# Kernel optimization log

Measured on AMD Instinct MI355X. Metric: run time of the kernel, lower is better.

Reference implementation:

```python
import jax, jax.numpy as jnp
import numpy as np

B, S, D, H = 8, 1024, 768, 12
DH = D // H  # per-head dim = 64


def setup_inputs() -> dict:
    key = jax.random.key(0)
    ks = jax.random.split(key, 9)
    scale = 1.0 / np.sqrt(D)
    x = jax.random.normal(ks[0], (B, S, D), dtype=jnp.float32)
    # Per-head projection weights stacked over the head axis [H, D, DH]
    Wq = jax.random.normal(ks[1], (H, D, DH), dtype=jnp.float32) * scale
    bq = jax.random.normal(ks[2], (H, DH), dtype=jnp.float32) * 0.02
    Wk = jax.random.normal(ks[3], (H, D, DH), dtype=jnp.float32) * scale
    bk = jax.random.normal(ks[4], (H, DH), dtype=jnp.float32) * 0.02
    Wv = jax.random.normal(ks[5], (H, D, DH), dtype=jnp.float32) * scale
    bv = jax.random.normal(ks[6], (H, DH), dtype=jnp.float32) * 0.02
    Wo = jax.random.normal(ks[7], (D, D), dtype=jnp.float32) * scale
    bo = jax.random.normal(ks[8], (D,), dtype=jnp.float32) * 0.02
    return {"x": x, "Wq": Wq, "bq": bq, "Wk": Wk, "bk": bk,
            "Wv": Wv, "bv": bv, "Wo": Wo, "bo": bo}


def reference(x, Wq, bq, Wk, bk, Wv, bv, Wo, bo):
    # Batched equivalent of the per-head Python loop: each head has its own
    # Q/K/V linear projections (weights stacked on the head axis).
    q = jnp.einsum('bsd,hde->bhse', x, Wq) + bq[None, :, None, :]
    k = jnp.einsum('bsd,hde->bhse', x, Wk) + bk[None, :, None, :]
    v = jnp.einsum('bsd,hde->bhse', x, Wv) + bv[None, :, None, :]
    scores = jnp.einsum('bhse,bhte->bhst', q, k) / jnp.sqrt(jnp.float32(DH))
    attn = jax.nn.softmax(scores, axis=-1)
    out = jnp.einsum('bhst,bhte->bhse', attn, v)  # [B,H,S,DH]
    # concat heads on last dim -> [B,S,H*DH] = [B,S,D]
    out = out.transpose(0, 2, 1, 3).reshape(B, S, D)
    return out @ Wo.T + bo
```

## Files before the change

### kernel.cpp

```cpp
#include <hip/hip_runtime.h>
#include <hip/hip_bf16.h>


typedef unsigned short u16;
typedef unsigned int u32;
typedef __attribute__((ext_vector_type(8))) short bf16x8;
typedef __attribute__((ext_vector_type(8))) unsigned short u16x8;
typedef __attribute__((ext_vector_type(4))) float f32x4;
typedef __attribute__((ext_vector_type(4))) u32 u32x4;

typedef __attribute__((address_space(1))) const u32* gas_u32;
typedef __attribute__((address_space(3))) u32* las_u32;

#define DEVI __device__ __forceinline__

DEVI u16 f2bf(float f) {
  union { float f; u32 u; } v; v.f = f;
  u32 r = v.u + 0x7fffu + ((v.u >> 16) & 1u);
  return (u16)(r >> 16);
}

DEVI void gll16(const void* g, void* l) {
  __builtin_amdgcn_global_load_lds((gas_u32)g, (las_u32)l, 16, 0, 0);
}

DEVI f32x4 mfma16(bf16x8 a, bf16x8 b, f32x4 c) {
  return __builtin_amdgcn_mfma_f32_16x16x32_bf16(a, b, c, 0, 0, 0);
}

DEVI u32 cvtpk(float lo, float hi) {
  u32 r;
  asm("v_cvt_pk_bf16_f32 %0, %1, %2" : "=v"(r) : "v"(lo), "v"(hi));
  return r;
}

__global__ __launch_bounds__(256) void k_prep(const float* __restrict__ x,
                                              u16* __restrict__ xb,
                                              const float* __restrict__ Wo,
                                              u16* __restrict__ Wob,
                                              const float* __restrict__ Wq,
                                              const float* __restrict__ Wk,
                                              const float* __restrict__ Wv,
                                              u16* __restrict__ Wtb) {
  __shared__ u16 T[64][65];
  const int blk = blockIdx.x;
  const int tid = threadIdx.x;
  if (blk < 6720) {
    const float* in; u16* out; int idx;
    if (blk < 6144) { in = x;  out = xb;  idx = blk * 256 + tid; }
    else            { in = Wo; out = Wob; idx = (blk - 6144) * 256 + tid; }
    float4 v = ((const float4*)in)[idx];
    ushort4 o;
    o.x = f2bf(v.x); o.y = f2bf(v.y); o.z = f2bf(v.z); o.w = f2bf(v.w);
    ((ushort4*)out)[idx] = o;
    return;
  }
  const int blk2 = blk - 6720;
  const int th = blk2 / 12;
  const int k0 = (blk2 % 12) * 64;
  const float* W = (th < 12) ? Wq : (th < 24) ? Wk : Wv;
  const int h = th % 12;
  W += (size_t)h * 768 * 64;
  const int row = tid >> 2, c = tid & 3;
  const float* src = W + (size_t)(k0 + row) * 64 + c * 16;
#pragma unroll
  for (int j = 0; j < 4; ++j) {
    float4 v = ((const float4*)src)[j];
    T[row][c * 16 + j * 4 + 0] = f2bf(v.x);
    T[row][c * 16 + j * 4 + 1] = f2bf(v.y);
    T[row][c * 16 + j * 4 + 2] = f2bf(v.z);
    T[row][c * 16 + j * 4 + 3] = f2bf(v.w);
  }
  __syncthreads();
  const int e = tid >> 2;
  u16* dst = Wtb + ((size_t)th * 64 + e) * 768 + k0 + c * 16;
  alignas(16) u16 tmp[16];
#pragma unroll
  for (int j = 0; j < 16; ++j) tmp[j] = T[c * 16 + j][e];
  *(u16x8*)(dst)     = *(const u16x8*)(tmp);
  *(u16x8*)(dst + 8) = *(const u16x8*)(tmp + 8);
}

__global__ __launch_bounds__(256) void k_gemmQKV(const u16* __restrict__ Ab,
                                                 const u16* __restrict__ Wtb,
                                                 const float* __restrict__ bq,
                                                 const float* __restrict__ bk,
                                                 const float* __restrict__ bv,
                                                 u16* __restrict__ Qb,
                                                 u16* __restrict__ VTb) {
  __shared__ u16 smem[12288];
  u16* As = smem;
  u16* Bs = smem + 128 * 64;
  const int tid = threadIdx.x;
  const int w = tid >> 6, lane = tid & 63, lq = lane & 15, g = lane >> 4;
  const int wm = w >> 1, wn = w & 1;
  const int m0 = blockIdx.x * 128;
  const int pn = blockIdx.y;
  const u16* Brows = Wtb + (size_t)pn * 64 * 768;

  f32x4 acc[4][2];
#pragma unroll
  for (int mf = 0; mf < 4; ++mf)
#pragma unroll
    for (int nf = 0; nf < 2; ++nf) acc[mf][nf] = (f32x4){0.f, 0.f, 0.f, 0.f};

  for (int kt = 0; kt < 12; ++kt) {
    const int kb = kt * 64;
#pragma unroll
    for (int i = 0; i < 4; ++i) {
      int c = w * 4 + i;
      int id = c * 64 + lane;
      int row = id >> 3, cb = id & 7;
      gll16(Ab + (size_t)(m0 + row) * 768 + kb + ((cb ^ (row & 7)) << 3), As + c * 512);
    }
#pragma unroll
    for (int i = 0; i < 2; ++i) {
      int c = w * 2 + i;
      int id = c * 64 + lane;
      int row = id >> 3, cb = id & 7;
      gll16(Brows + (size_t)row * 768 + kb + ((cb ^ (row & 7)) << 3), Bs + c * 512);
    }
    __syncthreads();
#pragma unroll
    for (int kk = 0; kk < 2; ++kk) {
      bf16x8 a[4], b[2];
#pragma unroll
      for (int mf = 0; mf < 4; ++mf) {
        int row = wm * 64 + mf * 16 + lq;
        a[mf] = *(const bf16x8*)(As + row * 64 + (((kk * 64 + g * 16) ^ ((row & 7) << 4)) >> 1));
      }
#pragma unroll
      for (int nf = 0; nf < 2; ++nf) {
        int row = wn * 32 + nf * 16 + lq;
        b[nf] = *(const bf16x8*)(Bs + row * 64 + (((kk * 64 + g * 16) ^ ((row & 7) << 4)) >> 1));
      }
#pragma unroll
      for (int mf = 0; mf < 4; ++mf)
#pragma unroll
        for (int nf = 0; nf < 2; ++nf)
          acc[mf][nf] = mfma16(a[mf], b[nf], acc[mf][nf]);
    }
    __syncthreads();
  }

  const int sel = pn / 12;
  const int ph  = pn % 12;
  const int b = m0 >> 10;
  if (sel == 2) {
    u16* Ct = smem;
#pragma unroll
    for (int nf = 0; nf < 2; ++nf) {
      const int e = wn * 32 + nf * 16 + lq;
      const float bi = bv[ph * 64 + e];
#pragma unroll
      for (int mf = 0; mf < 4; ++mf)
#pragma unroll
        for (int r = 0; r < 4; ++r) {
          int sl = wm * 64 + mf * 16 + 4 * g + r;
          Ct[e * 136 + sl] = f2bf(acc[mf][nf][r] + bi);
        }
    }
    __syncthreads();
    const int er = tid >> 2, cc = tid & 3;
    u16* dst = VTb + ((size_t)(b * 12 + ph) * 64 + er) * 1024 + (m0 & 1023) + cc * 32;
#pragma unroll
    for (int i = 0; i < 4; ++i)
      *(u16x8*)(dst + i * 8) = *(const u16x8*)(Ct + er * 136 + cc * 32 + i * 8);
  } else {
    u16* out = Qb + (size_t)sel * 6291456;
    const float qs = sel ? 1.0f : 0.18033688f;
    const float* bp = sel ? bk : bq;
#pragma unroll
    for (int nf = 0; nf < 2; ++nf) {
      const int e = wn * 32 + nf * 16 + lq;
      const float bi = bp[ph * 64 + e];
#pragma unroll
      for (int mf = 0; mf < 4; ++mf)
#pragma unroll
        for (int r = 0; r < 4; ++r) {
          int s = (m0 & 1023) + wm * 64 + mf * 16 + 4 * g + r;
          out[((size_t)(b * 12 + ph) * 1024 + s) * 64 + e] = f2bf((acc[mf][nf][r] + bi) * qs);
        }
    }
  }
}

__global__ __launch_bounds__(256) void k_gemmO(const u16* __restrict__ Ab,
                                               const u16* __restrict__ Bb,
                                               const float* __restrict__ bias,
                                               float* __restrict__ out) {
  __shared__ u16 smem[12288];
  u16* As = smem;
  u16* Bs = smem + 128 * 64;
  const int tid = threadIdx.x;
  const int w = tid >> 6, lane = tid & 63, lq = lane & 15, g = lane >> 4;
  const int wm = w >> 1, wn = w & 1;
  const int m0 = blockIdx.x * 128;
  const int pn = blockIdx.y;
  const u16* Brows = Bb + (size_t)pn * 64 * 768;

  f32x4 acc[4][2];
#pragma unroll
  for (int mf = 0; mf < 4; ++mf)
#pragma unroll
    for (int nf = 0; nf < 2; ++nf) acc[mf][nf] = (f32x4){0.f, 0.f, 0.f, 0.f};

  for (int kt = 0; kt < 12; ++kt) {
    const int kb = kt * 64;
#pragma unroll
    for (int i = 0; i < 4; ++i) {
      int c = w * 4 + i;
      int id = c * 64 + lane;
      int row = id >> 3, cb = id & 7;
      gll16(Ab + (size_t)(m0 + row) * 768 + kb + ((cb ^ (row & 7)) << 3), As + c * 512);
    }
#pragma unroll
    for (int i = 0; i < 2; ++i) {
      int c = w * 2 + i;
      int id = c * 64 + lane;
      int row = id >> 3, cb = id & 7;
      gll16(Brows + (size_t)row * 768 + kb + ((cb ^ (row & 7)) << 3), Bs + c * 512);
    }
    __syncthreads();
#pragma unroll
    for (int kk = 0; kk < 2; ++kk) {
      bf16x8 a[4], b[2];
#pragma unroll
      for (int mf = 0; mf < 4; ++mf) {
        int row = wm * 64 + mf * 16 + lq;
        a[mf] = *(const bf16x8*)(As + row * 64 + (((kk * 64 + g * 16) ^ ((row & 7) << 4)) >> 1));
      }
#pragma unroll
      for (int nf = 0; nf < 2; ++nf) {
        int row = wn * 32 + nf * 16 + lq;
        b[nf] = *(const bf16x8*)(Bs + row * 64 + (((kk * 64 + g * 16) ^ ((row & 7) << 4)) >> 1));
      }
#pragma unroll
      for (int mf = 0; mf < 4; ++mf)
#pragma unroll
        for (int nf = 0; nf < 2; ++nf)
          acc[mf][nf] = mfma16(a[mf], b[nf], acc[mf][nf]);
    }
    __syncthreads();
  }

#pragma unroll
  for (int nf = 0; nf < 2; ++nf) {
    const int n = pn * 64 + wn * 32 + nf * 16 + lq;
    const float bi = bias[n];
#pragma unroll
    for (int mf = 0; mf < 4; ++mf)
#pragma unroll
      for (int r = 0; r < 4; ++r) {
        int m = m0 + wm * 64 + mf * 16 + 4 * g + r;
        out[(size_t)m * 768 + n] = acc[mf][nf][r] + bi;
      }
  }
}

__global__ __launch_bounds__(512) void k_attn(const u16* __restrict__ Qb,
                                              const u16* __restrict__ Kb,
                                              const u16* __restrict__ VTb,
                                              u16* __restrict__ AO) {
  __shared__ u16 Ksm[2][4096];
  __shared__ u16 Vsm[2][4096];
  const int tid = threadIdx.x;
  const int w = tid >> 6, lane = tid & 63, lq = lane & 15, g = lane >> 4;
  const int bh = blockIdx.x, b = bh / 12, h = bh % 12;
  const int q0 = blockIdx.y * 128 + w * 16;
  const u16* Qw = Qb + ((size_t)bh * 1024 + q0) * 64;
  const u16* Kp = Kb + (size_t)bh * 65536;
  const u16* Vp = VTb + (size_t)bh * 65536;
  const bool gsel = (g & 1);

  bf16x8 qf[2];
#pragma unroll
  for (int kk = 0; kk < 2; ++kk)
    qf[kk] = *(const bf16x8*)(Qw + lq * 64 + kk * 32 + g * 8);

  f32x4 o[4];
#pragma unroll
  for (int ef = 0; ef < 4; ++ef) o[ef] = (f32x4){0.f, 0.f, 0.f, 0.f};
  float l_ = 0.f;

#define STAGE(buf, kt_)                                                          \
  {                                                                              \
    const int kb_ = (kt_) * 64;                                                  \
    const int id = w * 64 + lane;                                                \
    const int row = id >> 3, cb = id & 7;                                        \
    const int sb = cb ^ (row & 7);                                               \
    const int tb = (sb & 4) | ((sb & 1) << 1) | ((sb >> 1) & 1);                 \
    gll16(Kp + (size_t)(kb_ + row) * 64 + (sb << 3), &Ksm[buf][w * 512]);        \
    gll16(Vp + (size_t)row * 1024 + kb_ + (tb << 3), &Vsm[buf][w * 512]);        \
  }

#define TILE(buf)                                                                \
  {                                                                              \
    f32x4 s[4];                                                                  \
    _Pragma("unroll")                                                            \
    for (int kf = 0; kf < 4; ++kf) s[kf] = (f32x4){0.f, 0.f, 0.f, 0.f};          \
    __builtin_amdgcn_s_setprio(1);                                               \
    _Pragma("unroll")                                                            \
    for (int kf = 0; kf < 4; ++kf) {                                             \
      const int row = kf * 16 + lq;                                              \
      _Pragma("unroll")                                                          \
      for (int kk = 0; kk < 2; ++kk) {                                           \
        bf16x8 kfr = *(const bf16x8*)(&Ksm[buf][0] + row * 64 +                  \
                                      (((kk * 64 + g * 16) ^ ((row & 7) << 4)) >> 1)); \
        s[kf] = mfma16(kfr, qf[kk], s[kf]);                                      \
      }                                                                          \
    }                                                                            \
    __builtin_amdgcn_s_setprio(0);                                               \
    float sm = 0.f;                                                              \
    _Pragma("unroll")                                                            \
    for (int kf = 0; kf < 4; ++kf)                                               \
      _Pragma("unroll")                                                          \
      for (int r = 0; r < 4; ++r) {                                              \
        float p = __builtin_amdgcn_exp2f(s[kf][r]);                              \
        s[kf][r] = p;                                                            \
        sm += p;                                                                 \
      }                                                                          \
    l_ += sm;                                                                    \
    u32 D[4][2];                                                                 \
    _Pragma("unroll")                                                            \
    for (int kf = 0; kf < 4; ++kf) {                                             \
      D[kf][0] = cvtpk(s[kf][0], s[kf][1]);                                      \
      D[kf][1] = cvtpk(s[kf][2], s[kf][3]);                                      \
    }                                                                            \
    _Pragma("unroll")                                                            \
    for (int kk = 0; kk < 2; ++kk) {                                             \
      const int kk2 = kk * 2;                                                    \
      u32 sa0 = gsel ? D[kk2][0] : D[kk2 + 1][0];                                \
      u32 sa1 = gsel ? D[kk2][1] : D[kk2 + 1][1];                                \
      u32 xa0 = __shfl_xor(sa0, 16), xa1 = __shfl_xor(sa1, 16);                  \
      u32x4 t = { gsel ? xa0 : D[kk2][0],                                        \
                  gsel ? xa1 : D[kk2][1],                                        \
                  gsel ? D[kk2 + 1][0] : xa0,                                    \
                  gsel ? D[kk2 + 1][1] : xa1 };                                  \
      bf16x8 pb = __builtin_bit_cast(bf16x8, t);                                 \
      __builtin_amdgcn_s_setprio(1);                                             \
      _Pragma("unroll")                                                          \
      for (int ef = 0; ef < 4; ++ef) {                                           \
        const int row = ef * 16 + lq;                                            \
        bf16x8 vf = *(const bf16x8*)(&Vsm[buf][0] + row * 64 +                   \
                                     (((kk * 64 + g * 16) ^ ((row & 7) << 4)) >> 1)); \
        o[ef] = mfma16(vf, pb, o[ef]);                                           \
      }                                                                          \
      __builtin_amdgcn_s_setprio(0);                                             \
    }                                                                            \
  }

  STAGE(0, 0)
  asm volatile("s_waitcnt vmcnt(0)" ::: "memory");
  __syncthreads();

  for (int it = 0; it < 8; ++it) {
    const int kt = it * 2;
    STAGE(1, kt + 1)
    TILE(0)
    asm volatile("s_waitcnt vmcnt(0)" ::: "memory");
    __syncthreads();
    if (it < 7) STAGE(0, kt + 2)
    TILE(1)
    asm volatile("s_waitcnt vmcnt(0)" ::: "memory");
    __syncthreads();
  }

  l_ += __shfl_xor(l_, 16);
  l_ += __shfl_xor(l_, 32);

  const float inv = 1.0f / l_;
  u16* dst = AO + ((size_t)(b * 1024 + q0 + lq)) * 768 + h * 64 + g * 4;
#pragma unroll
  for (int ef = 0; ef < 4; ++ef) {
    ushort4 t;
    t.x = f2bf(o[ef][0] * inv);
    t.y = f2bf(o[ef][1] * inv);
    t.z = f2bf(o[ef][2] * inv);
    t.w = f2bf(o[ef][3] * inv);
    *(ushort4*)(dst + ef * 16) = t;
  }
#undef STAGE
#undef TILE
}

extern "C" void kernel_launch(void* const* d_in, const int* in_sizes, int n_in,
                              void* d_out, int out_size, void* d_ws, size_t ws_size,
                              hipStream_t stream) {
  (void)in_sizes; (void)n_in; (void)out_size; (void)ws_size;
  const float* x  = (const float*)d_in[0];
  const float* Wq = (const float*)d_in[1];
  const float* bq = (const float*)d_in[2];
  const float* Wk = (const float*)d_in[3];
  const float* bk = (const float*)d_in[4];
  const float* Wv = (const float*)d_in[5];
  const float* bv = (const float*)d_in[6];
  const float* Wo = (const float*)d_in[7];
  const float* bo = (const float*)d_in[8];

  char* ws = (char*)d_ws;
  u16* xb  = (u16*)(ws);
  u16* Wtb = (u16*)(ws + 12582912);
  u16* Wob = (u16*)(ws + 12582912 + 3538944);
  u16* Qb  = (u16*)(ws + 12582912 + 3538944 + 1179648);
  u16* Kb  = Qb + (size_t)96 * 1024 * 64;
  u16* VTb = Kb + (size_t)96 * 1024 * 64;
  u16* AO  = xb;

  k_prep<<<7152, 256, 0, stream>>>(x, xb, Wo, Wob, Wq, Wk, Wv, Wtb);

  k_gemmQKV<<<dim3(64, 36), 256, 0, stream>>>(xb, Wtb, bq, bk, bv, Qb, VTb);

  k_attn<<<dim3(96, 8), 512, 0, stream>>>(Qb, Kb, VTb, AO);

  k_gemmO<<<dim3(64, 12), 256, 0, stream>>>(AO, Wob, bo, (float*)d_out);
}
```

Before: 107.8 us.

## Double-buffer LDS tiles in QKV and output-projection GEMMs

Both projection GEMM kernels now keep two LDS stages and issue the async global-to-LDS loads for the next K tile before computing on the current one. This overlaps global memory latency with MFMA work and halves the barriers per K tile. In exchange, LDS per block doubles to 48KB, which may lower occupancy. The attention kernel is unchanged.

```diff
diff --git a/kernel.cpp b/kernel.cpp
--- a/kernel.cpp
+++ b/kernel.cpp
@@ -88,14 +88,13 @@
                                                  const float* __restrict__ bv,
                                                  u16* __restrict__ Qb,
                                                  u16* __restrict__ VTb) {
-  __shared__ u16 smem[12288];
-  u16* As = smem;
-  u16* Bs = smem + 128 * 64;
+  __shared__ u16 smem[2][12288];
   const int tid = threadIdx.x;
   const int w = tid >> 6, lane = tid & 63, lq = lane & 15, g = lane >> 4;
   const int wm = w >> 1, wn = w & 1;
   const int m0 = blockIdx.x * 128;
   const int pn = blockIdx.y;
+  const u16* Arows = Ab + (size_t)m0 * 768;
   const u16* Brows = Wtb + (size_t)pn * 64 * 768;
 
   f32x4 acc[4][2];
@@ -104,50 +103,76 @@
 #pragma unroll
     for (int nf = 0; nf < 2; ++nf) acc[mf][nf] = (f32x4){0.f, 0.f, 0.f, 0.f};
 
-  for (int kt = 0; kt < 12; ++kt) {
-    const int kb = kt * 64;
-#pragma unroll
-    for (int i = 0; i < 4; ++i) {
-      int c = w * 4 + i;
-      int id = c * 64 + lane;
-      int row = id >> 3, cb = id & 7;
-      gll16(Ab + (size_t)(m0 + row) * 768 + kb + ((cb ^ (row & 7)) << 3), As + c * 512);
-    }
-#pragma unroll
-    for (int i = 0; i < 2; ++i) {
-      int c = w * 2 + i;
-      int id = c * 64 + lane;
-      int row = id >> 3, cb = id & 7;
-      gll16(Brows + (size_t)row * 768 + kb + ((cb ^ (row & 7)) << 3), Bs + c * 512);
-    }
-    __syncthreads();
-#pragma unroll
-    for (int kk = 0; kk < 2; ++kk) {
-      bf16x8 a[4], b[2];
-#pragma unroll
-      for (int mf = 0; mf < 4; ++mf) {
-        int row = wm * 64 + mf * 16 + lq;
-        a[mf] = *(const bf16x8*)(As + row * 64 + (((kk * 64 + g * 16) ^ ((row & 7) << 4)) >> 1));
-      }
-#pragma unroll
-      for (int nf = 0; nf < 2; ++nf) {
-        int row = wn * 32 + nf * 16 + lq;
-        b[nf] = *(const bf16x8*)(Bs + row * 64 + (((kk * 64 + g * 16) ^ ((row & 7) << 4)) >> 1));
-      }
-#pragma unroll
-      for (int mf = 0; mf < 4; ++mf)
-#pragma unroll
-        for (int nf = 0; nf < 2; ++nf)
-          acc[mf][nf] = mfma16(a[mf], b[nf], acc[mf][nf]);
-    }
-    __syncthreads();
-  }
+#define QSTAGE(buf, kt_)                                                         \
+  {                                                                              \
+    const int kb_ = (kt_) * 64;                                                  \
+    _Pragma("unroll")                                                            \
+    for (int i = 0; i < 4; ++i) {                                                \
+      int c = w * 4 + i;                                                         \
+      int id = c * 64 + lane;                                                    \
+      int row = id >> 3, cb = id & 7;                                            \
+      gll16(Arows + (size_t)row * 768 + kb_ + ((cb ^ (row & 7)) << 3),           \
+            &smem[buf][c * 512]);                                                \
+    }                                                                            \
+    _Pragma("unroll")                                                            \
+    for (int i = 0; i < 2; ++i) {                                                \
+      int c = w * 2 + i;                                                         \
+      int id = c * 64 + lane;                                                    \
+      int row = id >> 3, cb = id & 7;                                            \
+      gll16(Brows + (size_t)row * 768 + kb_ + ((cb ^ (row & 7)) << 3),           \
+            &smem[buf][8192 + c * 512]);                                         \
+    }                                                                            \
+  }
+
+#define QCOMP(buf)                                                               \
+  {                                                                              \
+    const u16* As_ = &smem[buf][0];                                              \
+    const u16* Bs_ = &smem[buf][8192];                                           \
+    _Pragma("unroll")                                                            \
+    for (int kk = 0; kk < 2; ++kk) {                                             \
+      bf16x8 a[4], b[2];                                                         \
+      _Pragma("unroll")                                                          \
+      for (int mf = 0; mf < 4; ++mf) {                                           \
+        int row = wm * 64 + mf * 16 + lq;                                        \
+        a[mf] = *(const bf16x8*)(As_ + row * 64 +                                \
+                                 (((kk * 64 + g * 16) ^ ((row & 7) << 4)) >> 1)); \
+      }                                                                          \
+      _Pragma("unroll")                                                          \
+      for (int nf = 0; nf < 2; ++nf) {                                           \
+        int row = wn * 32 + nf * 16 + lq;                                        \
+        b[nf] = *(const bf16x8*)(Bs_ + row * 64 +                                \
+                                 (((kk * 64 + g * 16) ^ ((row & 7) << 4)) >> 1)); \
+      }                                                                          \
+      _Pragma("unroll")                                                          \
+      for (int mf = 0; mf < 4; ++mf)                                             \
+        _Pragma("unroll")                                                        \
+        for (int nf = 0; nf < 2; ++nf)                                           \
+          acc[mf][nf] = mfma16(a[mf], b[nf], acc[mf][nf]);                       \
+    }                                                                            \
+  }
+
+  QSTAGE(0, 0)
+  asm volatile("s_waitcnt vmcnt(0)" ::: "memory");
+  __syncthreads();
+  for (int it = 0; it < 6; ++it) {
+    const int kt = it * 2;
+    QSTAGE(1, kt + 1)
+    QCOMP(0)
+    asm volatile("s_waitcnt vmcnt(0)" ::: "memory");
+    __syncthreads();
+    if (it < 5) QSTAGE(0, kt + 2)
+    QCOMP(1)
+    asm volatile("s_waitcnt vmcnt(0)" ::: "memory");
+    __syncthreads();
+  }
+#undef QSTAGE
+#undef QCOMP
 
   const int sel = pn / 12;
   const int ph  = pn % 12;
   const int b = m0 >> 10;
   if (sel == 2) {
-    u16* Ct = smem;
+    u16* Ct = &smem[0][0];
 #pragma unroll
     for (int nf = 0; nf < 2; ++nf) {
       const int e = wn * 32 + nf * 16 + lq;
@@ -189,14 +214,13 @@
                                                const u16* __restrict__ Bb,
                                                const float* __restrict__ bias,
                                                float* __restrict__ out) {
-  __shared__ u16 smem[12288];
-  u16* As = smem;
-  u16* Bs = smem + 128 * 64;
+  __shared__ u16 smem[2][12288];
   const int tid = threadIdx.x;
   const int w = tid >> 6, lane = tid & 63, lq = lane & 15, g = lane >> 4;
   const int wm = w >> 1, wn = w & 1;
   const int m0 = blockIdx.x * 128;
   const int pn = blockIdx.y;
+  const u16* Arows = Ab + (size_t)m0 * 768;
   const u16* Brows = Bb + (size_t)pn * 64 * 768;
 
   f32x4 acc[4][2];
@@ -205,44 +229,70 @@
 #pragma unroll
     for (int nf = 0; nf < 2; ++nf) acc[mf][nf] = (f32x4){0.f, 0.f, 0.f, 0.f};
 
-  for (int kt = 0; kt < 12; ++kt) {
-    const int kb = kt * 64;
-#pragma unroll
-    for (int i = 0; i < 4; ++i) {
-      int c = w * 4 + i;
-      int id = c * 64 + lane;
-      int row = id >> 3, cb = id & 7;
-      gll16(Ab + (size_t)(m0 + row) * 768 + kb + ((cb ^ (row & 7)) << 3), As + c * 512);
-    }
-#pragma unroll
-    for (int i = 0; i < 2; ++i) {
-      int c = w * 2 + i;
-      int id = c * 64 + lane;
-      int row = id >> 3, cb = id & 7;
-      gll16(Brows + (size_t)row * 768 + kb + ((cb ^ (row & 7)) << 3), Bs + c * 512);
-    }
-    __syncthreads();
-#pragma unroll
-    for (int kk = 0; kk < 2; ++kk) {
-      bf16x8 a[4], b[2];
-#pragma unroll
-      for (int mf = 0; mf < 4; ++mf) {
-        int row = wm * 64 + mf * 16 + lq;
-        a[mf] = *(const bf16x8*)(As + row * 64 + (((kk * 64 + g * 16) ^ ((row & 7) << 4)) >> 1));
-      }
-#pragma unroll
-      for (int nf = 0; nf < 2; ++nf) {
-        int row = wn * 32 + nf * 16 + lq;
-        b[nf] = *(const bf16x8*)(Bs + row * 64 + (((kk * 64 + g * 16) ^ ((row & 7) << 4)) >> 1));
-      }
-#pragma unroll
-      for (int mf = 0; mf < 4; ++mf)
-#pragma unroll
-        for (int nf = 0; nf < 2; ++nf)
-          acc[mf][nf] = mfma16(a[mf], b[nf], acc[mf][nf]);
-    }
-    __syncthreads();
-  }
+#define OSTAGE(buf, kt_)                                                         \
+  {                                                                              \
+    const int kb_ = (kt_) * 64;                                                  \
+    _Pragma("unroll")                                                            \
+    for (int i = 0; i < 4; ++i) {                                                \
+      int c = w * 4 + i;                                                         \
+      int id = c * 64 + lane;                                                    \
+      int row = id >> 3, cb = id & 7;                                            \
+      gll16(Arows + (size_t)row * 768 + kb_ + ((cb ^ (row & 7)) << 3),           \
+            &smem[buf][c * 512]);                                                \
+    }                                                                            \
+    _Pragma("unroll")                                                            \
+    for (int i = 0; i < 2; ++i) {                                                \
+      int c = w * 2 + i;                                                         \
+      int id = c * 64 + lane;                                                    \
+      int row = id >> 3, cb = id & 7;                                            \
+      gll16(Brows + (size_t)row * 768 + kb_ + ((cb ^ (row & 7)) << 3),           \
+            &smem[buf][8192 + c * 512]);                                         \
+    }                                                                            \
+  }
+
+#define OCOMP(buf)                                                               \
+  {                                                                              \
+    const u16* As_ = &smem[buf][0];                                              \
+    const u16* Bs_ = &smem[buf][8192];                                           \
+    _Pragma("unroll")                                                            \
+    for (int kk = 0; kk < 2; ++kk) {                                             \
+      bf16x8 a[4], b[2];                                                         \
+      _Pragma("unroll")                                                          \
+      for (int mf = 0; mf < 4; ++mf) {                                           \
+        int row = wm * 64 + mf * 16 + lq;                                        \
+        a[mf] = *(const bf16x8*)(As_ + row * 64 +                                \
+                                 (((kk * 64 + g * 16) ^ ((row & 7) << 4)) >> 1)); \
+      }                                                                          \
+      _Pragma("unroll")                                                          \
+      for (int nf = 0; nf < 2; ++nf) {                                           \
+        int row = wn * 32 + nf * 16 + lq;                                        \
+        b[nf] = *(const bf16x8*)(Bs_ + row * 64 +                                \
+                                 (((kk * 64 + g * 16) ^ ((row & 7) << 4)) >> 1)); \
+      }                                                                          \
+      _Pragma("unroll")                                                          \
+      for (int mf = 0; mf < 4; ++mf)                                             \
+        _Pragma("unroll")                                                        \
+        for (int nf = 0; nf < 2; ++nf)                                           \
+          acc[mf][nf] = mfma16(a[mf], b[nf], acc[mf][nf]);                       \
+    }                                                                            \
+  }
+
+  OSTAGE(0, 0)
+  asm volatile("s_waitcnt vmcnt(0)" ::: "memory");
+  __syncthreads();
+  for (int it = 0; it < 6; ++it) {
+    const int kt = it * 2;
+    OSTAGE(1, kt + 1)
+    OCOMP(0)
+    asm volatile("s_waitcnt vmcnt(0)" ::: "memory");
+    __syncthreads();
+    if (it < 5) OSTAGE(0, kt + 2)
+    OCOMP(1)
+    asm volatile("s_waitcnt vmcnt(0)" ::: "memory");
+    __syncthreads();
+  }
+#undef OSTAGE
+#undef OCOMP
 
 #pragma unroll
   for (int nf = 0; nf < 2; ++nf) {
```

Measured after the change: 106.8 us. No clear change (-0.9%).
